# Kernel tuning notes

Measured on AMD Instinct MI355X. Metric: run time of the kernel, lower is better.

The kernel has to match this reference:

```python
import jax, jax.numpy as jnp
import numpy as np

N_NODES = 100000
NUM_ETYPE = 4
HEADS = 4
HID = 32
IN_CH = 128
EDGE_CH = 32
N_EDGES = 800000
BATCH = 1024
NEG = 5


def setup_inputs() -> dict:
    key = jax.random.key(0)
    ks = jax.random.split(key, 24)

    def w(k, shape, s=0.05):
        return jax.random.normal(k, shape, dtype=jnp.float32) * s

    inp = {}
    inp["edge_index"] = jax.random.randint(ks[0], (2, N_EDGES), 0, N_NODES)
    inp["edge_type"] = jax.random.randint(ks[1], (N_EDGES,), 0, NUM_ETYPE)
    inp["n_id"] = jax.random.randint(ks[2], (BATCH * (2 + NEG),), 0, N_NODES)
    inp["neg_sample_num"] = NEG
    inp["id_emb"] = w(ks[3], (N_NODES, IN_CH), 0.1)
    dims = [IN_CH, HEADS * HID]
    for i in range(2):
        d_in = dims[i]
        base = 4 + i * 7
        inp[f"W{i}"] = w(ks[base], (d_in, HEADS * HID))
        inp[f"Wres{i}"] = w(ks[base + 1], (d_in, HEADS * HID))
        inp[f"al{i}"] = w(ks[base + 2], (HEADS, HID))
        inp[f"ar{i}"] = w(ks[base + 3], (HEADS, HID))
        inp[f"ae{i}"] = w(ks[base + 4], (HEADS, EDGE_CH))
        inp[f"eemb{i}"] = w(ks[base + 5], (NUM_ETYPE, EDGE_CH))
        inp[f"We{i}"] = w(ks[base + 6], (EDGE_CH, HEADS * EDGE_CH))
    inp["pW1"] = w(ks[18], (2 * HEADS * HID, HID))
    inp["pb1"] = jnp.zeros((HID,), jnp.float32)
    inp["pW2"] = w(ks[19], (HID, 1))
    inp["pb2"] = jnp.zeros((1,), jnp.float32)
    return inp


def _leaky(x):
    return jnp.where(x > 0, x, 0.2 * x)  # LeakyReLU(0.2)


def _conv(h, src, dst, etype, W, Wres, al, ar, ae, eemb, We):
    """Simple-HGN style edge-typed graph attention conv with linear residual."""
    n = h.shape[0]
    feat = (h @ W).reshape(n, HEADS, HID)                      # [N,H,D]
    ef = (eemb @ We).reshape(NUM_ETYPE, HEADS, EDGE_CH)        # [T,H,De]
    el = jnp.einsum('nhd,hd->nh', feat, al)                    # [N,H]
    er = jnp.einsum('nhd,hd->nh', feat, ar)                    # [N,H]
    ee = jnp.einsum('thd,hd->th', ef, ae)                      # [T,H]
    logits = _leaky(el[src] + er[dst] + ee[etype])             # [E,H]
    # numerically stable per-destination softmax over incoming edges
    m = jax.ops.segment_max(logits, dst, num_segments=n)
    m = jnp.where(jnp.isfinite(m), m, jnp.zeros_like(m))
    a = jnp.exp(logits - m[dst])
    denom = jax.ops.segment_sum(a, dst, num_segments=n)
    alpha = a / (denom[dst] + 1e-16)                           # [E,H]
    out = jax.ops.segment_sum(feat[src] * alpha[:, :, None], dst, num_segments=n)
    return out.reshape(n, HEADS * HID) + h @ Wres


def reference(edge_index, edge_type, n_id, neg_sample_num, id_emb,
              W0, Wres0, al0, ar0, ae0, eemb0, We0,
              W1, Wres1, al1, ar1, ae1, eemb1, We1,
              pW1, pb1, pW2, pb2):
    src, dst = edge_index[0], edge_index[1]
    x = _conv(id_emb, src, dst, edge_type, W0, Wres0, al0, ar0, ae0, eemb0, We0)
    x = jax.nn.relu(x)  # relu between layers; dropout inactive at eval
    x = _conv(x, src, dst, edge_type, W1, Wres1, al1, ar1, ae1, eemb1, We1)
    b = n_id.shape[0] // (2 + neg_sample_num)
    out = x[n_id[:b]]
    pos = x[n_id[b:2 * b]]
    neg = x[n_id[2 * b:]]
    tiled = jnp.repeat(out, neg_sample_num, axis=0)  # repeat(1,neg).reshape(-1,D)

    def head(z):
        return _leaky(z @ pW1 + pb1) @ pW2 + pb2

    pos_logit = head(jnp.concatenate([out, pos], axis=-1))
    neg_logits = head(jnp.concatenate([tiled, neg], axis=-1))
    return pos_logit, neg_logits
```

## Files before the change

kernel.cpp:

```cpp
#include <hip/hip_runtime.h>
#include <hip/hip_bf16.h>
#include <math.h>

#define HEADS 4
#define HID 32
#define DIM 128
#define NEGS 5

typedef short s16x8 __attribute__((ext_vector_type(8)));
typedef short s16x4 __attribute__((ext_vector_type(4)));
typedef unsigned short u16x8 __attribute__((ext_vector_type(8)));
typedef float f32x4 __attribute__((ext_vector_type(4)));

__device__ __forceinline__ unsigned short f2bf_rn(float x) {
    unsigned int u = __float_as_uint(x);
    unsigned int r = (u + 0x7FFFu + ((u >> 16) & 1u)) >> 16;
    return (unsigned short)r;
}
__device__ __forceinline__ float bf2f(unsigned short b) {
    return __uint_as_float(((unsigned int)b) << 16);
}

__global__ void k_hist(const int* __restrict__ dst, int* __restrict__ counts, int E) {
    int e = blockIdx.x * 256 + threadIdx.x;
    if (e < E) atomicAdd(&counts[dst[e]], 1);
}

__global__ __launch_bounds__(1024) void k_scanA(const int* __restrict__ counts,
                                                int* __restrict__ rowtmp,
                                                int* __restrict__ bsum, int N) {
    __shared__ int s[1024];
    int i = blockIdx.x * 1024 + threadIdx.x;
    int v = (i < N) ? counts[i] : 0;
    s[threadIdx.x] = v;
    __syncthreads();
    for (int off = 1; off < 1024; off <<= 1) {
        int t = (threadIdx.x >= off) ? s[threadIdx.x - off] : 0;
        __syncthreads();
        s[threadIdx.x] += t;
        __syncthreads();
    }
    if (i < N) rowtmp[i] = s[threadIdx.x];
    if (threadIdx.x == 1023) bsum[blockIdx.x] = s[1023];
}

__global__ void k_scanB(const int* __restrict__ bsum, int* __restrict__ bsumex, int nb) {
    int l = threadIdx.x;
    int a = (2 * l < nb) ? bsum[2 * l] : 0;
    int b = (2 * l + 1 < nb) ? bsum[2 * l + 1] : 0;
    int s = a + b;
    for (int off = 1; off < 64; off <<= 1) {
        int t = __shfl_up(s, off);
        if (l >= off) s += t;
    }
    int excl = s - (a + b);
    if (2 * l < nb) bsumex[2 * l] = excl;
    if (2 * l + 1 < nb) bsumex[2 * l + 1] = excl + a;
}

__global__ void k_scanC(const int* __restrict__ rowtmp, const int* __restrict__ counts,
                        const int* __restrict__ bsumex, int* __restrict__ row_start,
                        int* __restrict__ cursor, int N) {
    int i = blockIdx.x * 256 + threadIdx.x;
    if (i < N) {
        int st = rowtmp[i] - counts[i] + bsumex[i >> 10];
        row_start[i] = st;
        cursor[i] = st;
    }
}

__global__ void k_scatter(const int* __restrict__ dst, int* __restrict__ cursor,
                          int* __restrict__ csr_edge, int E) {
    int e = blockIdx.x * 256 + threadIdx.x;
    if (e < E) {
        int p = atomicAdd(&cursor[dst[e]], 1);
        csr_edge[p] = e;
    }
}

__global__ void k_flag2(const int* __restrict__ n_id, int* __restrict__ flag2,
                        int* __restrict__ flag1, int M) {
    int i = blockIdx.x * 256 + threadIdx.x;
    if (i < M) { int n = n_id[i]; flag2[n] = 1; flag1[n] = 1; }
}

__global__ void k_flag1(const int* __restrict__ src, const int* __restrict__ dst,
                        const int* __restrict__ flag2, int* __restrict__ flag1, int E) {
    int e = blockIdx.x * 256 + threadIdx.x;
    if (e < E && flag2[dst[e]]) flag1[src[e]] = 1;
}

__global__ void k_compact(const int* __restrict__ flag1, const int* __restrict__ flag2,
                          int* __restrict__ list1, int* __restrict__ list2,
                          int* __restrict__ cnt1, int* __restrict__ cnt2, int N) {
    int i = blockIdx.x * 256 + threadIdx.x;
    int lane = threadIdx.x & 63;
    unsigned long long lt = (lane == 63) ? ~0ull >> 1 : (1ull << lane) - 1;

    bool a = (i < N) && flag1[i];
    unsigned long long m = __ballot(a);
    int base = 0;
    if (lane == 0 && m) base = atomicAdd(cnt1, __popcll(m));
    base = __shfl(base, 0);
    if (a) list1[base + __popcll(m & lt)] = i;

    bool b = (i < N) && flag2[i];
    m = __ballot(b);
    base = 0;
    if (lane == 0 && m) base = atomicAdd(cnt2, __popcll(m));
    base = __shfl(base, 0);
    if (b) list2[base + __popcll(m & lt)] = i;
}

__global__ void k_wcvt(const float* __restrict__ W0, const float* __restrict__ Wres0,
                       const float* __restrict__ W1, const float* __restrict__ Wres1,
                       unsigned short* __restrict__ bt) {
    int idx = blockIdx.x * 256 + threadIdx.x;
    int layer = idx >> 15;
    int r = idx & 32767;
    int k = r >> 8;
    int n = r & 255;
    const float* src = layer ? ((n < 128) ? W1 : Wres1) : ((n < 128) ? W0 : Wres0);
    float x = src[k * 128 + (n & 127)];
    unsigned short h = f2bf_rn(x);
    unsigned short l = f2bf_rn(x - bf2f(h));
    unsigned short* base = bt + (size_t)layer * 2 * 32768;
    base[n * 128 + k] = h;
    base[32768 + n * 128 + k] = l;
}

__global__ __launch_bounds__(256, 4) void k_gemm_mfma(const float* __restrict__ A,
                                                      const unsigned short* __restrict__ Bhi,
                                                      const unsigned short* __restrict__ Blo,
                                                      float* __restrict__ feat,
                                                      float* __restrict__ res,
                                                      const int* __restrict__ rowlist,
                                                      const int* __restrict__ rowcnt,
                                                      int N) {
    int limit = rowcnt ? *rowcnt : N;
    int m0 = blockIdx.y * 64;
    if (m0 >= limit) return;

    __shared__ unsigned short Bh[8192];
    __shared__ unsigned short Bl[8192];
    int tid = threadIdx.x;
    int n0 = blockIdx.x * 64;

#pragma unroll
    for (int i = 0; i < 4; ++i) {
        int c = tid + i * 256;
        int row = c >> 4, g16 = c & 15;
        int off = (row * 256 + ((g16 * 16) ^ ((row & 7) << 4))) >> 1;
        *(u16x8*)&Bh[off] = *(const u16x8*)(Bhi + (size_t)(n0 + row) * DIM + g16 * 8);
        *(u16x8*)&Bl[off] = *(const u16x8*)(Blo + (size_t)(n0 + row) * DIM + g16 * 8);
    }

    int lane = tid & 63, w = tid >> 6;
    int wm = (w & 1) * 32, wn = (w >> 1) * 32;
    int lr = lane & 15, g = lane >> 4;

    s16x8 afh[2][4], afl[2][4];
#pragma unroll
    for (int fm = 0; fm < 2; ++fm) {
        int idx = m0 + wm + fm * 16 + lr;
        bool valid = idx < limit;
        int grow = 0;
        if (valid) grow = rowlist ? rowlist[idx] : idx;
        const float* ap = A + (size_t)grow * DIM;
#pragma unroll
        for (int ks = 0; ks < 4; ++ks) {
            float4 p = make_float4(0.f, 0.f, 0.f, 0.f);
            float4 q = make_float4(0.f, 0.f, 0.f, 0.f);
            if (valid) {
                p = *(const float4*)(ap + ks * 32 + g * 4);
                q = *(const float4*)(ap + ks * 32 + 16 + g * 4);
            }
            float vv[8] = {p.x, p.y, p.z, p.w, q.x, q.y, q.z, q.w};
            s16x8 hv, lv;
#pragma unroll
            for (int j = 0; j < 8; ++j) {
                unsigned short h = f2bf_rn(vv[j]);
                hv[j] = (short)h;
                lv[j] = (short)f2bf_rn(vv[j] - bf2f(h));
            }
            afh[fm][ks] = hv;
            afl[fm][ks] = lv;
        }
    }
    __syncthreads();

    f32x4 acc[2][2];
#pragma unroll
    for (int fm = 0; fm < 2; ++fm)
#pragma unroll
        for (int fn = 0; fn < 2; ++fn) acc[fm][fn] = (f32x4){0.f, 0.f, 0.f, 0.f};

#pragma unroll
    for (int ks = 0; ks < 4; ++ks) {
        s16x8 bfh[2], bfl[2];
#pragma unroll
        for (int fn = 0; fn < 2; ++fn) {
            int row = wn + fn * 16 + lr;
            int sw = (row & 7) << 4;
            int o1 = (row * 256 + ((ks * 64 + g * 8) ^ sw)) >> 1;
            int o2 = (row * 256 + ((ks * 64 + 32 + g * 8) ^ sw)) >> 1;
            s16x4 p = *(const s16x4*)&Bh[o1];
            s16x4 q = *(const s16x4*)&Bh[o2];
            bfh[fn] = (s16x8){p[0], p[1], p[2], p[3], q[0], q[1], q[2], q[3]};
            p = *(const s16x4*)&Bl[o1];
            q = *(const s16x4*)&Bl[o2];
            bfl[fn] = (s16x8){p[0], p[1], p[2], p[3], q[0], q[1], q[2], q[3]};
        }
#pragma unroll
        for (int fm = 0; fm < 2; ++fm)
#pragma unroll
            for (int fn = 0; fn < 2; ++fn) {
                acc[fm][fn] = __builtin_amdgcn_mfma_f32_16x16x32_bf16(afh[fm][ks], bfh[fn], acc[fm][fn], 0, 0, 0);
                acc[fm][fn] = __builtin_amdgcn_mfma_f32_16x16x32_bf16(afh[fm][ks], bfl[fn], acc[fm][fn], 0, 0, 0);
                acc[fm][fn] = __builtin_amdgcn_mfma_f32_16x16x32_bf16(afl[fm][ks], bfh[fn], acc[fm][fn], 0, 0, 0);
            }
    }

#pragma unroll
    for (int fm = 0; fm < 2; ++fm)
#pragma unroll
        for (int fn = 0; fn < 2; ++fn) {
            int idx0 = m0 + wm + fm * 16 + g * 4;
            int gc = n0 + wn + fn * 16 + lr;
            float* dp = (gc < 128) ? feat : res;
            int dc = gc & 127;
#pragma unroll
            for (int r = 0; r < 4; ++r) {
                int idx = idx0 + r;
                if (idx < limit) {
                    int gr = rowlist ? rowlist[idx] : idx;
                    dp[(size_t)gr * DIM + dc] = acc[fm][fn][r];
                }
            }
        }
}

__global__ void k_elr(const float* __restrict__ feat, const float* __restrict__ al,
                      const float* __restrict__ ar, float* __restrict__ el,
                      float* __restrict__ er, const int* __restrict__ list,
                      const int* __restrict__ cnt, int N) {
    int limit = cnt ? *cnt : N;
    int t = blockIdx.x * 256 + threadIdx.x;
    if (t >= limit * HEADS) return;
    int idx = t >> 2, h = t & 3;
    int node = list ? list[idx] : idx;
    const float4* f = (const float4*)(feat + (size_t)node * DIM + h * HID);
    const float4* Ap = (const float4*)(al + h * HID);
    const float4* Rp = (const float4*)(ar + h * HID);
    float sl = 0.f, sr = 0.f;
#pragma unroll
    for (int d = 0; d < 8; ++d) {
        float4 v = f[d], a = Ap[d], r = Rp[d];
        sl += v.x * a.x + v.y * a.y + v.z * a.z + v.w * a.w;
        sr += v.x * r.x + v.y * r.y + v.z * r.z + v.w * r.w;
    }
    el[node * 4 + h] = sl;
    er[node * 4 + h] = sr;
}

__global__ void k_ee(const float* __restrict__ eemb, const float* __restrict__ We,
                     const float* __restrict__ ae, float* __restrict__ ee) {
    int t = threadIdx.x;
    if (t >= 16) return;
    int et = t >> 2, h = t & 3;
    float s = 0.f;
    for (int d = 0; d < 32; ++d) {
        float ef = 0.f;
        for (int k = 0; k < 32; ++k) ef += eemb[et * 32 + k] * We[k * DIM + h * 32 + d];
        s += ef * ae[h * 32 + d];
    }
    ee[t] = s;
}

template <int RELU>
__global__ __launch_bounds__(256) void k_agg(const float* __restrict__ feat,
                                             const float* __restrict__ el,
                                             const float* __restrict__ er,
                                             const float* __restrict__ eeB,
                                             const int* __restrict__ srcArr,
                                             const int* __restrict__ etArr,
                                             const int* __restrict__ csr_edge,
                                             const int* __restrict__ row_start,
                                             const int* __restrict__ counts,
                                             const int* __restrict__ dlist,
                                             const int* __restrict__ dcnt,
                                             float* __restrict__ out) {
    int wv = threadIdx.x >> 6;
    int lane = threadIdx.x & 63;
    int idx = blockIdx.x * 4 + wv;
    if (idx >= *dcnt) return;
    int node = dlist[idx];

    int beg = row_start[node];
    int deg = counts[node];
    int eh = lane & 3;
    float er_v = er[node * 4 + eh];

    float m = -INFINITY;
    for (int base = 0; base < deg; base += 16) {
        int ei = base + (lane >> 2);
        float lg = -INFINITY;
        if (ei < deg) {
            int e = csr_edge[beg + ei];
            float x = el[srcArr[e] * 4 + eh] + er_v + eeB[etArr[e] * 4 + eh];
            lg = (x > 0.f) ? x : 0.2f * x;
        }
        m = fmaxf(m, lg);
    }
    for (int off = 4; off < 64; off <<= 1) m = fmaxf(m, __shfl_xor(m, off));

    float denom = 0.f, acc0 = 0.f, acc1 = 0.f;
    int h1 = lane >> 5;
    for (int base = 0; base < deg; base += 16) {
        int ei = base + (lane >> 2);
        float wgt = 0.f;
        int s = 0;
        if (ei < deg) {
            int e = csr_edge[beg + ei];
            s = srcArr[e];
            float x = el[s * 4 + eh] + er_v + eeB[etArr[e] * 4 + eh];
            x = (x > 0.f) ? x : 0.2f * x;
            wgt = expf(x - m);
            denom += wgt;
        }
        int cnt = min(16, deg - base);
        for (int j = 0; j < cnt; ++j) {
            int sj = __shfl(s, j * 4);
            float w1 = __shfl(wgt, j * 4 + h1);
            float w2 = __shfl(wgt, j * 4 + 2 + h1);
            acc0 += w1 * feat[(size_t)sj * DIM + lane];
            acc1 += w2 * feat[(size_t)sj * DIM + 64 + lane];
        }
    }
    for (int off = 4; off < 64; off <<= 1) denom += __shfl_xor(denom, off);
    float d1 = __shfl(denom, h1);
    float d2 = __shfl(denom, 2 + h1);

    float r0 = out[(size_t)node * DIM + lane] + acc0 / (d1 + 1e-16f);
    float r1 = out[(size_t)node * DIM + 64 + lane] + acc1 / (d2 + 1e-16f);
    if (RELU) { r0 = fmaxf(r0, 0.f); r1 = fmaxf(r1, 0.f); }
    out[(size_t)node * DIM + lane] = r0;
    out[(size_t)node * DIM + 64 + lane] = r1;
}

__global__ __launch_bounds__(256) void k_head(const float* __restrict__ x1,
                                              const int* __restrict__ n_id,
                                              const float* __restrict__ pW1,
                                              const float* __restrict__ pb1,
                                              const float* __restrict__ pW2,
                                              const float* __restrict__ pb2,
                                              float* __restrict__ dout, int B) {
    int o = blockIdx.x * 4 + (threadIdx.x >> 6);
    int lane = threadIdx.x & 63;
    int total = B + B * NEGS;
    if (o >= total) return;
    int a, c;
    if (o < B) { a = n_id[o]; c = n_id[B + o]; }
    else { int j = o - B; a = n_id[j / NEGS]; c = n_id[2 * B + j]; }

    int j = lane & 31;
    int half = lane >> 5;
    int row = half ? c : a;
    const float* z = x1 + (size_t)row * DIM;
    const float* w = pW1 + (half ? 128 * 32 : 0);
    float t = 0.f;
#pragma unroll 8
    for (int k = 0; k < 128; ++k) t += z[k] * w[k * 32 + j];
    t += __shfl_xor(t, 32);
    t += pb1[j];
    t = (t > 0.f) ? t : 0.2f * t;
    float r = t * pW2[j];
    for (int off = 1; off < 32; off <<= 1) r += __shfl_xor(r, off);
    if (lane == 0) dout[o] = r + pb2[0];
}

extern "C" void kernel_launch(void* const* d_in, const int* in_sizes, int n_in,
                              void* d_out, int out_size, void* d_ws, size_t ws_size,
                              hipStream_t stream) {
    const int* edge_index = (const int*)d_in[0];
    const int* etype      = (const int*)d_in[1];
    const int* n_id       = (const int*)d_in[2];
    const float* id_emb   = (const float*)d_in[4];
    const float* W0    = (const float*)d_in[5];
    const float* Wres0 = (const float*)d_in[6];
    const float* al0   = (const float*)d_in[7];
    const float* ar0   = (const float*)d_in[8];
    const float* ae0   = (const float*)d_in[9];
    const float* eemb0 = (const float*)d_in[10];
    const float* We0   = (const float*)d_in[11];
    const float* W1    = (const float*)d_in[12];
    const float* Wres1 = (const float*)d_in[13];
    const float* al1   = (const float*)d_in[14];
    const float* ar1   = (const float*)d_in[15];
    const float* ae1   = (const float*)d_in[16];
    const float* eemb1 = (const float*)d_in[17];
    const float* We1   = (const float*)d_in[18];
    const float* pW1   = (const float*)d_in[19];
    const float* pb1   = (const float*)d_in[20];
    const float* pW2   = (const float*)d_in[21];
    const float* pb2   = (const float*)d_in[22];

    int E = in_sizes[1];
    int N = in_sizes[4] / DIM;
    int M = in_sizes[2];
    int B = M / (2 + NEGS);
    const int* srcArr = edge_index;
    const int* dstArr = edge_index + E;

    size_t N128 = (size_t)N * DIM;
    float* feat = (float*)d_ws;
    float* x0   = feat + N128;
    float* x1   = x0 + N128;
    float* el   = x1 + N128;
    float* er   = el + (size_t)N * 4;
    float* eeB  = er + (size_t)N * 4;
    int* counts    = (int*)(eeB + 32);
    int* flag1     = counts + N;
    int* flag2     = flag1 + N;
    int* cnt1      = flag2 + N;
    int* cnt2      = cnt1 + 1;
    int* rowtmp    = cnt2 + 1;
    int* row_start = rowtmp + N;
    int* cursor    = row_start + N;
    int* csr_edge  = cursor + N;
    int* list1     = csr_edge + E;
    int* list2     = list1 + N;
    int* bsum      = list2 + M;
    int* bsumex    = bsum + 256;
    unsigned short* bt = (unsigned short*)(bsumex + 256);

    k_wcvt<<<256, 256, 0, stream>>>(W0, Wres0, W1, Wres1, bt);
    hipMemsetAsync(counts, 0, (size_t)(3 * N + 2) * sizeof(int), stream);

    k_hist<<<(E + 255) / 256, 256, 0, stream>>>(dstArr, counts, E);
    int nb = (N + 1023) / 1024;
    k_scanA<<<nb, 1024, 0, stream>>>(counts, rowtmp, bsum, N);
    k_scanB<<<1, 64, 0, stream>>>(bsum, bsumex, nb);
    k_scanC<<<(N + 255) / 256, 256, 0, stream>>>(rowtmp, counts, bsumex, row_start, cursor, N);
    k_scatter<<<(E + 255) / 256, 256, 0, stream>>>(dstArr, cursor, csr_edge, E);

    k_flag2<<<(M + 255) / 256, 256, 0, stream>>>(n_id, flag2, flag1, M);
    k_flag1<<<(E + 255) / 256, 256, 0, stream>>>(srcArr, dstArr, flag2, flag1, E);
    k_compact<<<(N + 255) / 256, 256, 0, stream>>>(flag1, flag2, list1, list2, cnt1, cnt2, N);

    dim3 ggrid(4, (N + 63) / 64);
    int aggGridFull = (N + 3) / 4;
    int aggGridS2 = (M + 3) / 4;

    k_gemm_mfma<<<ggrid, 256, 0, stream>>>(id_emb, bt, bt + 32768, feat, x0,
                                           nullptr, nullptr, N);
    k_elr<<<(N * HEADS + 255) / 256, 256, 0, stream>>>(feat, al0, ar0, el, er,
                                                       nullptr, nullptr, N);
    k_ee<<<1, 16, 0, stream>>>(eemb0, We0, ae0, eeB);
    k_agg<1><<<aggGridFull, 256, 0, stream>>>(feat, el, er, eeB, srcArr, etype, csr_edge,
                                              row_start, counts, list1, cnt1, x0);

    k_gemm_mfma<<<ggrid, 256, 0, stream>>>(x0, bt + 65536, bt + 98304, feat, x1,
                                           list1, cnt1, N);
    k_elr<<<(N * HEADS + 255) / 256, 256, 0, stream>>>(feat, al1, ar1, el, er,
                                                       list1, cnt1, N);
    k_ee<<<1, 16, 0, stream>>>(eemb1, We1, ae1, eeB);
    k_agg<0><<<aggGridS2, 256, 0, stream>>>(feat, el, er, eeB, srcArr, etype, csr_edge,
                                            row_start, counts, list2, cnt2, x1);

    int total = B * (1 + NEGS);
    k_head<<<(total + 3) / 4, 256, 0, stream>>>(x1, n_id, pW1, pb1, pW2, pb2,
                                                (float*)d_out, B);
}
```

Measured before the change: 402.5 us.

## Fuse el/er dot products into GEMM epilogue and merge histogram with frontier flagging

The GEMM now gives each block a 64-row tile and loops over all four 64-column chunks of the weight matrix. The A fragments are loaded and converted to bf16 hi/lo once instead of four times. The per-head attention dot products el/er are computed in the epilogue with lane shuffles, which removes the separate k_elr pass that re-read feat. The edge histogram and the layer-1 frontier flagging are merged into one edge pass, saving a kernel launch and a re-read of dst. In exchange there are fewer GEMM blocks, B tiles are reloaded serially with extra syncthreads, and shuffle reductions are added.

```diff
diff --git a/kernel.cpp b/kernel.cpp
--- a/kernel.cpp
+++ b/kernel.cpp
@@ -21,9 +21,15 @@
     return __uint_as_float(((unsigned int)b) << 16);
 }
 
-__global__ void k_hist(const int* __restrict__ dst, int* __restrict__ counts, int E) {
+__global__ void k_histflag(const int* __restrict__ src, const int* __restrict__ dst,
+                           const int* __restrict__ flag2,
+                           int* __restrict__ counts, int* __restrict__ flag1, int E) {
     int e = blockIdx.x * 256 + threadIdx.x;
-    if (e < E) atomicAdd(&counts[dst[e]], 1);
+    if (e < E) {
+        int d = dst[e];
+        atomicAdd(&counts[d], 1);
+        if (flag2[d]) flag1[src[e]] = 1;
+    }
 }
 
 __global__ __launch_bounds__(1024) void k_scanA(const int* __restrict__ counts,
@@ -82,12 +88,6 @@
                         int* __restrict__ flag1, int M) {
     int i = blockIdx.x * 256 + threadIdx.x;
     if (i < M) { int n = n_id[i]; flag2[n] = 1; flag1[n] = 1; }
-}
-
-__global__ void k_flag1(const int* __restrict__ src, const int* __restrict__ dst,
-                        const int* __restrict__ flag2, int* __restrict__ flag1, int E) {
-    int e = blockIdx.x * 256 + threadIdx.x;
-    if (e < E && flag2[dst[e]]) flag1[src[e]] = 1;
 }
 
 __global__ void k_compact(const int* __restrict__ flag1, const int* __restrict__ flag2,
@@ -129,32 +129,25 @@
     base[32768 + n * 128 + k] = l;
 }
 
-__global__ __launch_bounds__(256, 4) void k_gemm_mfma(const float* __restrict__ A,
-                                                      const unsigned short* __restrict__ Bhi,
-                                                      const unsigned short* __restrict__ Blo,
-                                                      float* __restrict__ feat,
-                                                      float* __restrict__ res,
-                                                      const int* __restrict__ rowlist,
-                                                      const int* __restrict__ rowcnt,
-                                                      int N) {
+__global__ __launch_bounds__(256, 4) void k_gemm_fused(const float* __restrict__ A,
+                                                       const unsigned short* __restrict__ Bhi,
+                                                       const unsigned short* __restrict__ Blo,
+                                                       float* __restrict__ feat,
+                                                       float* __restrict__ res,
+                                                       const float* __restrict__ al,
+                                                       const float* __restrict__ ar,
+                                                       float* __restrict__ el,
+                                                       float* __restrict__ er,
+                                                       const int* __restrict__ rowlist,
+                                                       const int* __restrict__ rowcnt,
+                                                       int N) {
     int limit = rowcnt ? *rowcnt : N;
-    int m0 = blockIdx.y * 64;
+    int m0 = blockIdx.x * 64;
     if (m0 >= limit) return;
 
     __shared__ unsigned short Bh[8192];
     __shared__ unsigned short Bl[8192];
     int tid = threadIdx.x;
-    int n0 = blockIdx.x * 64;
-
-#pragma unroll
-    for (int i = 0; i < 4; ++i) {
-        int c = tid + i * 256;
-        int row = c >> 4, g16 = c & 15;
-        int off = (row * 256 + ((g16 * 16) ^ ((row & 7) << 4))) >> 1;
-        *(u16x8*)&Bh[off] = *(const u16x8*)(Bhi + (size_t)(n0 + row) * DIM + g16 * 8);
-        *(u16x8*)&Bl[off] = *(const u16x8*)(Blo + (size_t)(n0 + row) * DIM + g16 * 8);
-    }
-
     int lane = tid & 63, w = tid >> 6;
     int wm = (w & 1) * 32, wn = (w >> 1) * 32;
     int lr = lane & 15, g = lane >> 4;
@@ -187,80 +180,94 @@
             afl[fm][ks] = lv;
         }
     }
-    __syncthreads();
-
-    f32x4 acc[2][2];
-#pragma unroll
-    for (int fm = 0; fm < 2; ++fm)
-#pragma unroll
-        for (int fn = 0; fn < 2; ++fn) acc[fm][fn] = (f32x4){0.f, 0.f, 0.f, 0.f};
-
-#pragma unroll
-    for (int ks = 0; ks < 4; ++ks) {
-        s16x8 bfh[2], bfl[2];
-#pragma unroll
-        for (int fn = 0; fn < 2; ++fn) {
-            int row = wn + fn * 16 + lr;
-            int sw = (row & 7) << 4;
-            int o1 = (row * 256 + ((ks * 64 + g * 8) ^ sw)) >> 1;
-            int o2 = (row * 256 + ((ks * 64 + 32 + g * 8) ^ sw)) >> 1;
-            s16x4 p = *(const s16x4*)&Bh[o1];
-            s16x4 q = *(const s16x4*)&Bh[o2];
-            bfh[fn] = (s16x8){p[0], p[1], p[2], p[3], q[0], q[1], q[2], q[3]};
-            p = *(const s16x4*)&Bl[o1];
-            q = *(const s16x4*)&Bl[o2];
-            bfl[fn] = (s16x8){p[0], p[1], p[2], p[3], q[0], q[1], q[2], q[3]};
-        }
+
+    for (int c = 0; c < 4; ++c) {
+#pragma unroll
+        for (int i = 0; i < 4; ++i) {
+            int f = tid + i * 256;
+            int row = f >> 4, g16 = f & 15;
+            int off = (row * 256 + ((g16 * 16) ^ ((row & 7) << 4))) >> 1;
+            *(u16x8*)&Bh[off] = *(const u16x8*)(Bhi + (size_t)(c * 64 + row) * DIM + g16 * 8);
+            *(u16x8*)&Bl[off] = *(const u16x8*)(Blo + (size_t)(c * 64 + row) * DIM + g16 * 8);
+        }
+        __syncthreads();
+
+        f32x4 acc[2][2];
 #pragma unroll
         for (int fm = 0; fm < 2; ++fm)
 #pragma unroll
+            for (int fn = 0; fn < 2; ++fn) acc[fm][fn] = (f32x4){0.f, 0.f, 0.f, 0.f};
+
+#pragma unroll
+        for (int ks = 0; ks < 4; ++ks) {
+            s16x8 bfh[2], bfl[2];
+#pragma unroll
             for (int fn = 0; fn < 2; ++fn) {
-                acc[fm][fn] = __builtin_amdgcn_mfma_f32_16x16x32_bf16(afh[fm][ks], bfh[fn], acc[fm][fn], 0, 0, 0);
-                acc[fm][fn] = __builtin_amdgcn_mfma_f32_16x16x32_bf16(afh[fm][ks], bfl[fn], acc[fm][fn], 0, 0, 0);
-                acc[fm][fn] = __builtin_amdgcn_mfma_f32_16x16x32_bf16(afl[fm][ks], bfh[fn], acc[fm][fn], 0, 0, 0);
+                int row = wn + fn * 16 + lr;
+                int sw = (row & 7) << 4;
+                int o1 = (row * 256 + ((ks * 64 + g * 8) ^ sw)) >> 1;
+                int o2 = (row * 256 + ((ks * 64 + 32 + g * 8) ^ sw)) >> 1;
+                s16x4 p = *(const s16x4*)&Bh[o1];
+                s16x4 q = *(const s16x4*)&Bh[o2];
+                bfh[fn] = (s16x8){p[0], p[1], p[2], p[3], q[0], q[1], q[2], q[3]};
+                p = *(const s16x4*)&Bl[o1];
+                q = *(const s16x4*)&Bl[o2];
+                bfl[fn] = (s16x8){p[0], p[1], p[2], p[3], q[0], q[1], q[2], q[3]};
             }
-    }
-
-#pragma unroll
-    for (int fm = 0; fm < 2; ++fm)
-#pragma unroll
-        for (int fn = 0; fn < 2; ++fn) {
-            int idx0 = m0 + wm + fm * 16 + g * 4;
-            int gc = n0 + wn + fn * 16 + lr;
-            float* dp = (gc < 128) ? feat : res;
-            int dc = gc & 127;
-#pragma unroll
-            for (int r = 0; r < 4; ++r) {
-                int idx = idx0 + r;
-                if (idx < limit) {
-                    int gr = rowlist ? rowlist[idx] : idx;
-                    dp[(size_t)gr * DIM + dc] = acc[fm][fn][r];
+#pragma unroll
+            for (int fm = 0; fm < 2; ++fm)
+#pragma unroll
+                for (int fn = 0; fn < 2; ++fn) {
+                    acc[fm][fn] = __builtin_amdgcn_mfma_f32_16x16x32_bf16(afh[fm][ks], bfh[fn], acc[fm][fn], 0, 0, 0);
+                    acc[fm][fn] = __builtin_amdgcn_mfma_f32_16x16x32_bf16(afh[fm][ks], bfl[fn], acc[fm][fn], 0, 0, 0);
+                    acc[fm][fn] = __builtin_amdgcn_mfma_f32_16x16x32_bf16(afl[fm][ks], bfh[fn], acc[fm][fn], 0, 0, 0);
+                }
+        }
+
+        float* dp = (c < 2) ? feat : res;
+#pragma unroll
+        for (int fm = 0; fm < 2; ++fm)
+#pragma unroll
+            for (int fn = 0; fn < 2; ++fn) {
+                int idx0 = m0 + wm + fm * 16 + g * 4;
+                int dc = ((c * 64) & 127) + wn + fn * 16 + lr;
+#pragma unroll
+                for (int r = 0; r < 4; ++r) {
+                    int idx = idx0 + r;
+                    if (idx < limit) {
+                        int gr = rowlist ? rowlist[idx] : idx;
+                        dp[(size_t)gr * DIM + dc] = acc[fm][fn][r];
+                    }
                 }
             }
-        }
-}
-
-__global__ void k_elr(const float* __restrict__ feat, const float* __restrict__ al,
-                      const float* __restrict__ ar, float* __restrict__ el,
-                      float* __restrict__ er, const int* __restrict__ list,
-                      const int* __restrict__ cnt, int N) {
-    int limit = cnt ? *cnt : N;
-    int t = blockIdx.x * 256 + threadIdx.x;
-    if (t >= limit * HEADS) return;
-    int idx = t >> 2, h = t & 3;
-    int node = list ? list[idx] : idx;
-    const float4* f = (const float4*)(feat + (size_t)node * DIM + h * HID);
-    const float4* Ap = (const float4*)(al + h * HID);
-    const float4* Rp = (const float4*)(ar + h * HID);
-    float sl = 0.f, sr = 0.f;
-#pragma unroll
-    for (int d = 0; d < 8; ++d) {
-        float4 v = f[d], a = Ap[d], r = Rp[d];
-        sl += v.x * a.x + v.y * a.y + v.z * a.z + v.w * a.w;
-        sr += v.x * r.x + v.y * r.y + v.z * r.z + v.w * r.w;
-    }
-    el[node * 4 + h] = sl;
-    er[node * 4 + h] = sr;
+
+        if (c < 2) {
+            int h = c * 2 + (wn >> 5);
+            float a0 = al[h * HID + lr], a1 = al[h * HID + 16 + lr];
+            float b0 = ar[h * HID + lr], b1 = ar[h * HID + 16 + lr];
+#pragma unroll
+            for (int fm = 0; fm < 2; ++fm)
+#pragma unroll
+                for (int r = 0; r < 4; ++r) {
+                    float ev = acc[fm][0][r] * a0 + acc[fm][1][r] * a1;
+                    float rv = acc[fm][0][r] * b0 + acc[fm][1][r] * b1;
+#pragma unroll
+                    for (int off = 1; off < 16; off <<= 1) {
+                        ev += __shfl_xor(ev, off);
+                        rv += __shfl_xor(rv, off);
+                    }
+                    if (lr == 0) {
+                        int idx = m0 + wm + fm * 16 + g * 4 + r;
+                        if (idx < limit) {
+                            int node = rowlist ? rowlist[idx] : idx;
+                            el[node * 4 + h] = ev;
+                            er[node * 4 + h] = rv;
+                        }
+                    }
+                }
+        }
+        __syncthreads();
+    }
 }
 
 __global__ void k_ee(const float* __restrict__ eemb, const float* __restrict__ We,
@@ -437,33 +444,28 @@
     k_wcvt<<<256, 256, 0, stream>>>(W0, Wres0, W1, Wres1, bt);
     hipMemsetAsync(counts, 0, (size_t)(3 * N + 2) * sizeof(int), stream);
 
-    k_hist<<<(E + 255) / 256, 256, 0, stream>>>(dstArr, counts, E);
+    k_flag2<<<(M + 255) / 256, 256, 0, stream>>>(n_id, flag2, flag1, M);
+    k_histflag<<<(E + 255) / 256, 256, 0, stream>>>(srcArr, dstArr, flag2, counts, flag1, E);
+
     int nb = (N + 1023) / 1024;
     k_scanA<<<nb, 1024, 0, stream>>>(counts, rowtmp, bsum, N);
     k_scanB<<<1, 64, 0, stream>>>(bsum, bsumex, nb);
     k_scanC<<<(N + 255) / 256, 256, 0, stream>>>(rowtmp, counts, bsumex, row_start, cursor, N);
     k_scatter<<<(E + 255) / 256, 256, 0, stream>>>(dstArr, cursor, csr_edge, E);
-
-    k_flag2<<<(M + 255) / 256, 256, 0, stream>>>(n_id, flag2, flag1, M);
-    k_flag1<<<(E + 255) / 256, 256, 0, stream>>>(srcArr, dstArr, flag2, flag1, E);
     k_compact<<<(N + 255) / 256, 256, 0, stream>>>(flag1, flag2, list1, list2, cnt1, cnt2, N);
 
-    dim3 ggrid(4, (N + 63) / 64);
+    int nRowBlk = (N + 63) / 64;
     int aggGridFull = (N + 3) / 4;
     int aggGridS2 = (M + 3) / 4;
 
-    k_gemm_mfma<<<ggrid, 256, 0, stream>>>(id_emb, bt, bt + 32768, feat, x0,
-                                           nullptr, nullptr, N);
-    k_elr<<<(N * HEADS + 255) / 256, 256, 0, stream>>>(feat, al0, ar0, el, er,
-                                                       nullptr, nullptr, N);
+    k_gemm_fused<<<nRowBlk, 256, 0, stream>>>(id_emb, bt, bt + 32768, feat, x0,
+                                              al0, ar0, el, er, nullptr, nullptr, N);
     k_ee<<<1, 16, 0, stream>>>(eemb0, We0, ae0, eeB);
     k_agg<1><<<aggGridFull, 256, 0, stream>>>(feat, el, er, eeB, srcArr, etype, csr_edge,
                                               row_start, counts, list1, cnt1, x0);
 
-    k_gemm_mfma<<<ggrid, 256, 0, stream>>>(x0, bt + 65536, bt + 98304, feat, x1,
-                                           list1, cnt1, N);
-    k_elr<<<(N * HEADS + 255) / 256, 256, 0, stream>>>(feat, al1, ar1, el, er,
-                                                       list1, cnt1, N);
+    k_gemm_fused<<<nRowBlk, 256, 0, stream>>>(x0, bt + 65536, bt + 98304, feat, x1,
+                                              al1, ar1, el, er, list1, cnt1, N);
     k_ee<<<1, 16, 0, stream>>>(eemb1, We1, ae1, eeB);
     k_agg<0><<<aggGridS2, 256, 0, stream>>>(feat, el, er, eeB, srcArr, etype, csr_edge,
                                             row_start, counts, list2, cnt2, x1);
```

Measured after the change: 427.6 us. 6.2% more time.
